# Kernel tuning notes

Hardware: AMD Instinct MI355X
Metric: run time of the kernel (lower is better)

## Reference

```python
import math
import jax, jax.numpy as jnp
import numpy as np

B = 8192
BAND = 5      # channels per DGCN
N = 62        # graph nodes (EEG electrodes)
LAYERS = 2
CBAM_C = (LAYERS + 1) * BAND  # 15
RED = 4
H2 = 64
K_TOP = int(N * 0.8)  # 49


def conv1x1(x, w, b):
    # x: [B,C,N,T], w: [O,C], b: [O] or None
    y = jnp.einsum('bcnt,oc->bont', x, w)
    if b is not None:
        y = y + b[None, :, None, None]
    return y


def dgcn(x, conv_w, conv_b, mem, gfc_w, gfc_b, gcn_w, gcn_b):
    skip = x
    x = conv1x1(x, conv_w, conv_b)
    scale = 1.0 / math.sqrt(BAND)
    # dynamic adjacency 1: memory-based
    a1 = jax.nn.softmax(jax.nn.relu(jnp.einsum('bcnt,cm->bnm', x, mem) * scale), axis=-1)
    # dynamic adjacency 2: self-similarity of time-summed features
    xs = jnp.sum(x, axis=-1)  # [B,C,N]
    a2 = jax.nn.softmax(jax.nn.relu(jnp.einsum('bcn,bcm->bnm', xs, xs) * scale), axis=-1)
    af = jnp.stack([a1, a2], axis=-1)          # [B,N,N,2]
    af = jnp.einsum('bnmk,ok->bnmo', af, gfc_w)[..., 0] + gfc_b[0]  # fc(2->1), squeeze
    af = jax.nn.softmax(af, axis=-1)
    _, idx = jax.lax.top_k(af, K_TOP)          # [B,N,k]
    bI = jnp.arange(af.shape[0])[:, None, None]
    nI = jnp.arange(N)[None, :, None]
    mask = jnp.zeros_like(af).at[bI, nI, idx].set(1.0)
    adj = af * mask
    # diffusion step (diffusion_step=1)
    y = jnp.einsum('bcnt,bnm->bcmt', x, adj)
    y = conv1x1(y, gcn_w, gcn_b)
    return y + skip


def cbam(x, ca_w1, ca_w2, sa_w, sa_b):
    residual = x
    # channel attention: shared SE MLP on max- and avg-pooled descriptors
    mx = jnp.max(x, axis=(2, 3), keepdims=True)   # [B,C,1,1]
    av = jnp.mean(x, axis=(2, 3), keepdims=True)
    def se(z):
        z = jnp.einsum('bcnt,oc->bont', z, ca_w1)
        z = jax.nn.relu(z)
        return jnp.einsum('bcnt,oc->bont', z, ca_w2)
    ca = jax.nn.sigmoid(se(mx) + se(av))
    out = x * ca
    # spatial attention: 3x3 conv over [max,mean] channel maps
    smax = jnp.max(out, axis=1, keepdims=True)
    smean = jnp.mean(out, axis=1, keepdims=True)
    s = jnp.concatenate([smax, smean], axis=1)    # [B,2,H,W]
    sa = jax.lax.conv_general_dilated(
        s, sa_w, window_strides=(1, 1), padding=((1, 1), (1, 1)),
        dimension_numbers=('NCHW', 'OIHW', 'NCHW')) + sa_b[None, :, None, None]
    sa = jax.nn.sigmoid(sa)
    out = out * sa
    return out + residual


def setup_inputs() -> dict:
    key = jax.random.key(0)
    ks = jax.random.split(key, 24)
    p = {}
    p['x'] = jax.random.normal(ks[0], (B, BAND * N), dtype=jnp.float32)
    for l in range(LAYERS):
        o = 1 + l * 8
        p[f'l{l}_conv_w'] = jax.random.normal(ks[o + 0], (BAND, BAND), jnp.float32) * 0.3
        p[f'l{l}_conv_b'] = jnp.zeros((BAND,), jnp.float32)
        p[f'l{l}_mem'] = jax.random.normal(ks[o + 1], (BAND, N), jnp.float32) * 0.2
        p[f'l{l}_gfc_w'] = jax.random.normal(ks[o + 2], (1, 2), jnp.float32) * 0.5
        p[f'l{l}_gfc_b'] = jnp.zeros((1,), jnp.float32)
        p[f'l{l}_gcn_w'] = jax.random.normal(ks[o + 3], (BAND, BAND), jnp.float32) * 0.3
        p[f'l{l}_gcn_b'] = jnp.zeros((BAND,), jnp.float32)
    p['ca_w1'] = jax.random.normal(ks[17], (CBAM_C // RED, CBAM_C), jnp.float32) * 0.2
    p['ca_w2'] = jax.random.normal(ks[18], (CBAM_C, CBAM_C // RED), jnp.float32) * 0.2
    p['sa_w'] = jax.random.normal(ks[19], (1, 2, 3, 3), jnp.float32) * 0.2
    p['sa_b'] = jnp.zeros((1,), jnp.float32)
    p['fc1_w'] = jax.random.normal(ks[20], (H2, N * CBAM_C), jnp.float32) * 0.03
    p['fc1_b'] = jnp.zeros((H2,), jnp.float32)
    p['fc2_w'] = jax.random.normal(ks[21], (H2, H2), jnp.float32) * 0.1
    p['fc2_b'] = jnp.zeros((H2,), jnp.float32)
    return p


def reference(x,
              l0_conv_w, l0_conv_b, l0_mem, l0_gfc_w, l0_gfc_b, l0_gcn_w, l0_gcn_b,
              l1_conv_w, l1_conv_b, l1_mem, l1_gfc_w, l1_gfc_b, l1_gcn_w, l1_gcn_b,
              ca_w1, ca_w2, sa_w, sa_b, fc1_w, fc1_b, fc2_w, fc2_b):
    h = x.reshape(x.shape[0], BAND, N)[:, :, :, None]  # [B,5,62,1]
    feats = [h]
    layer_params = [
        (l0_conv_w, l0_conv_b, l0_mem, l0_gfc_w, l0_gfc_b, l0_gcn_w, l0_gcn_b),
        (l1_conv_w, l1_conv_b, l1_mem, l1_gfc_w, l1_gfc_b, l1_gcn_w, l1_gcn_b),
    ]
    cur = h
    for lp in layer_params:
        cur = dgcn(cur, *lp)
        feats.append(cur)
    g = jnp.concatenate(feats, axis=1)                 # [B,15,62,1]
    g = cbam(g, ca_w1, ca_w2, sa_w, sa_b)
    out = g.reshape(g.shape[0], -1)
    out = jax.nn.relu(out @ fc1_w.T + fc1_b)           # dropout = identity (eval)
    out = jax.nn.relu(out @ fc2_w.T + fc2_b)
    return out
```

## Files before the change

### kernel.cpp

```cpp
#include <hip/hip_runtime.h>

#define NB 62
#define NC 5
#define KTOP 49

typedef unsigned short ushort_t;
typedef unsigned int uint_t;

__device__ __forceinline__ float sigmf(float x) {
    return 1.0f / (1.0f + __expf(-x));
}

__device__ __forceinline__ ushort_t f2b(float f) {
    union { float f; uint_t u; } cv; cv.f = f;
    uint_t r = (cv.u + 0x7fffu + ((cv.u >> 16) & 1u)) >> 16;
    return (ushort_t)r;
}
__device__ __forceinline__ float blo(uint_t w) {
    union { uint_t u; float f; } cv; cv.u = w << 16; return cv.f;
}
__device__ __forceinline__ float bhi(uint_t w) {
    union { uint_t u; float f; } cv; cv.u = w & 0xffff0000u; return cv.f;
}
__device__ __forceinline__ float bits2f(uint_t u) {
    union { uint_t u; float f; } cv; cv.u = u; return cv.f;
}

__device__ __forceinline__ float tmax31(const float* a) {
    float t0 = a[0], t1 = a[1], t2 = a[2], t3 = a[3];
    #pragma unroll
    for (int m = 4; m < 28; m += 4) {
        t0 = fmaxf(t0, a[m]);     t1 = fmaxf(t1, a[m + 1]);
        t2 = fmaxf(t2, a[m + 2]); t3 = fmaxf(t3, a[m + 3]);
    }
    t0 = fmaxf(t0, a[28]); t1 = fmaxf(t1, a[29]); t2 = fmaxf(t2, a[30]);
    return fmaxf(fmaxf(t0, t1), fmaxf(t2, t3));
}
__device__ __forceinline__ float tsum31(const float* a) {
    float t0 = a[0], t1 = a[1], t2 = a[2], t3 = a[3];
    #pragma unroll
    for (int m = 4; m < 28; m += 4) {
        t0 += a[m]; t1 += a[m + 1]; t2 += a[m + 2]; t3 += a[m + 3];
    }
    t0 += a[28]; t1 += a[29]; t2 += a[30];
    return (t0 + t1) + (t2 + t3);
}

__device__ __forceinline__ void sort16(float* s) {
    #pragma unroll
    for (int k = 2; k <= 16; k <<= 1) {
        #pragma unroll
        for (int j = k >> 1; j > 0; j >>= 1) {
            #pragma unroll
            for (int i = 0; i < 16; ++i) {
                const int p = i ^ j;
                if (p > i) {
                    const bool up = ((i & k) == 0);
                    const float a = s[i], c = s[p];
                    s[i] = up ? fminf(a, c) : fmaxf(a, c);
                    s[p] = up ? fmaxf(a, c) : fminf(a, c);
                }
            }
        }
    }
}
__device__ __forceinline__ void merge_low16(float* m, const float* b) {
    float t[16];
    #pragma unroll
    for (int i = 0; i < 16; ++i) t[i] = fminf(m[i], b[15 - i]);
    #pragma unroll
    for (int j = 8; j > 0; j >>= 1) {
        #pragma unroll
        for (int i = 0; i < 16; ++i) {
            const int p = i ^ j;
            if (p > i) {
                const float a = t[i], c = t[p];
                t[i] = fminf(a, c);
                t[p] = fmaxf(a, c);
            }
        }
    }
    #pragma unroll
    for (int i = 0; i < 16; ++i) m[i] = t[i];
}

__global__ void repack_kernel(const float* __restrict__ fc1w,
                              const float* __restrict__ fc2w,
                              ushort_t* __restrict__ w1o,
                              float* __restrict__ w2o) {
    const int i = blockIdx.x * 256 + threadIdx.x;
    if (i < 59 * 128 * 8) {
        const int e = i & 7, t = (i >> 3) & 127, j = i >> 10;
        const int o = t >> 1, h = t & 1;
        const int f = (h * 59 + j) * 8 + e;
        const float v = (f < 930) ? fc1w[o * 930 + f] : 0.0f;
        w1o[i] = f2b(v);
    } else if (i < 59 * 128 * 8 + 8 * 128 * 4) {
        const int i2 = i - 59 * 128 * 8;
        const int e = i2 & 3, t = (i2 >> 2) & 127, j = i2 >> 9;
        const int o = t >> 1, h = t & 1;
        w2o[i2] = fc2w[o * 64 + h * 32 + j * 4 + e];
    }
}

template <int L>
__device__ __forceinline__ void dgcn_layer(
    const int tid, const float* __restrict__ xin_g,
    const float* __restrict__ conv_w, const float* __restrict__ conv_b,
    const float* __restrict__ memp,
    const float* __restrict__ gfc_w, const float* __restrict__ gfc_b,
    const float* __restrict__ gcn_w, const float* __restrict__ gcn_b,
    float (*__restrict__ s_xc4)[4], float* __restrict__ s_xc1,
    float (*__restrict__ s_me4)[4], float* __restrict__ s_me1,
    uint_t* __restrict__ s_adj32,
    float (*__restrict__ s_xin)[NC], float (*__restrict__ s_xout)[NC])
{
    const float scale = 0.44721359549995793f;
    const int n = tid >> 1, h = tid & 1;

    for (int i = tid; i < NC * NB; i += 128) {
        const int c = i / NB, m = i - c * NB;
        if (c < 4) s_me4[m][c] = memp[i];
        else       s_me1[m]    = memp[i];
    }

    if (tid < NB) {
        float cw[25], cbv[5];
        #pragma unroll
        for (int i = 0; i < 25; ++i) cw[i] = conv_w[i];
        #pragma unroll
        for (int i = 0; i < 5; ++i)  cbv[i] = conv_b[i];
        float xn[5];
        #pragma unroll
        for (int c = 0; c < 5; ++c)
            xn[c] = (L == 0) ? xin_g[c * NB + tid] : s_xin[tid][c];
        float xo[5];
        #pragma unroll
        for (int o = 0; o < 5; ++o) {
            float a = cbv[o];
            #pragma unroll
            for (int c = 0; c < 5; ++c) a = fmaf(cw[o * 5 + c], xn[c], a);
            xo[o] = a;
        }
        s_xc4[tid][0] = xo[0]; s_xc4[tid][1] = xo[1];
        s_xc4[tid][2] = xo[2]; s_xc4[tid][3] = xo[3];
        s_xc1[tid] = xo[4];
    }
    __syncthreads();

    if (n < NB) {
        const float w0 = gfc_w[0], w1 = gfc_w[1], b0 = gfc_b[0];
        const float4 xo03 = *(const float4*)&s_xc4[n][0];
        const float  xo4  = s_xc1[n];
        float r1[31], r2[31];
        #pragma unroll
        for (int i = 0; i < 31; ++i) {
            const int m = h * 31 + i;
            const float4 xc03 = *(const float4*)&s_xc4[m][0];
            const float  xc4  = s_xc1[m];
            const float4 me03 = *(const float4*)&s_me4[m][0];
            const float  me4  = s_me1[m];
            float s1 = xo03.x * me03.x + xo03.y * me03.y + xo03.z * me03.z +
                       xo03.w * me03.w + xo4 * me4;
            float s2 = xo03.x * xc03.x + xo03.y * xc03.y + xo03.z * xc03.z +
                       xo03.w * xc03.w + xo4 * xc4;
            r1[i] = fmaxf(s1 * scale, 0.0f);
            r2[i] = fmaxf(s2 * scale, 0.0f);
        }
        float mx1 = tmax31(r1);
        mx1 = fmaxf(mx1, __shfl_xor(mx1, 1, 64));
        #pragma unroll
        for (int i = 0; i < 31; ++i) r1[i] = __expf(r1[i] - mx1);
        float sm1 = tsum31(r1);
        sm1 += __shfl_xor(sm1, 1, 64);
        const float inv1 = 1.0f / sm1;
        float mx2 = tmax31(r2);
        mx2 = fmaxf(mx2, __shfl_xor(mx2, 1, 64));
        #pragma unroll
        for (int i = 0; i < 31; ++i) r2[i] = __expf(r2[i] - mx2);
        float sm2 = tsum31(r2);
        sm2 += __shfl_xor(sm2, 1, 64);
        const float inv2 = 1.0f / sm2;
        #pragma unroll
        for (int i = 0; i < 31; ++i)
            r1[i] = b0 + (r1[i] * inv1) * w0 + (r2[i] * inv2) * w1;
        float mxa = tmax31(r1);
        mxa = fmaxf(mxa, __shfl_xor(mxa, 1, 64));
        #pragma unroll
        for (int i = 0; i < 31; ++i) r1[i] = __expf(r1[i] - mxa);
        float sma = tsum31(r1);
        sma += __shfl_xor(sma, 1, 64);
        const float inva = 1.0f / sma;
        #pragma unroll
        for (int i = 0; i < 31; ++i) r1[i] *= inva;

        float ga[16], gb[16];
        #pragma unroll
        for (int i = 0; i < 16; ++i) ga[i] = r1[i];
        sort16(ga);
        #pragma unroll
        for (int i = 0; i < 15; ++i) gb[i] = r1[16 + i];
        gb[15] = INFINITY;
        sort16(gb);
        merge_low16(ga, gb);
        #pragma unroll
        for (int i = 0; i < 16; ++i) gb[i] = __shfl_xor(ga[i], 1, 64);
        merge_low16(ga, gb);
        const float vth = ga[13];

        int g_own = 0, eq_own = 0;
        #pragma unroll
        for (int i = 0; i < 31; ++i) {
            g_own  += (r1[i] > vth);
            eq_own += (r1[i] == vth);
        }
        const int G = g_own + __shfl_xor(g_own, 1, 64);
        const int eq_other = __shfl_xor(eq_own, 1, 64);
        int eq = h ? eq_other : 0;

        uint_t pend = 0, myfirst = 0;
        #pragma unroll
        for (int i = 0; i < 31; ++i) {
            const bool e  = (r1[i] == vth);
            const bool ss = (r1[i] > vth) || (e && (G + eq) < KTOP);
            const uint_t hb = (uint_t)f2b(ss ? r1[i] : 0.0f);
            eq += e ? 1 : 0;
            if (h == 0) {
                if (i & 1) s_adj32[n * 31 + (i >> 1)] = pend | (hb << 16);
                else       pend = hb;
            } else {
                if (i == 0)      myfirst = hb;
                else if (i & 1)  pend = hb;
                else             s_adj32[n * 31 + 15 + (i >> 1)] = pend | (hb << 16);
            }
        }
        const uint_t xch = (uint_t)__shfl_xor((int)(h ? myfirst : pend), 1, 64);
        if (h == 0) s_adj32[n * 31 + 15] = pend | (xch << 16);
    }
    __syncthreads();

    if (n < NB) {
        const int m = n;
        const int dw = m >> 1;
        const uint_t sh = (m & 1) ? 16u : 0u;
        float y0 = 0, y1 = 0, y2 = 0, y3 = 0, y4 = 0;
        #pragma unroll 4
        for (int j = 0; j < 31; ++j) {
            const int nn = h * 31 + j;
            const uint_t w = s_adj32[nn * 31 + dw];
            const float a = bits2f((w >> sh) << 16);
            const float4 xv = *(const float4*)&s_xc4[nn][0];
            const float  xv4 = s_xc1[nn];
            y0 = fmaf(xv.x, a, y0); y1 = fmaf(xv.y, a, y1); y2 = fmaf(xv.z, a, y2);
            y3 = fmaf(xv.w, a, y3); y4 = fmaf(xv4, a, y4);
        }
        y0 += __shfl_xor(y0, 1, 64); y1 += __shfl_xor(y1, 1, 64);
        y2 += __shfl_xor(y2, 1, 64); y3 += __shfl_xor(y3, 1, 64);
        y4 += __shfl_xor(y4, 1, 64);
        if (h == 0) {
            float gwv[25], gbv[5];
            #pragma unroll
            for (int i = 0; i < 25; ++i) gwv[i] = gcn_w[i];
            #pragma unroll
            for (int i = 0; i < 5; ++i)  gbv[i] = gcn_b[i];
            #pragma unroll
            for (int o = 0; o < 5; ++o) {
                const float z = gbv[o] + gwv[o * 5 + 0] * y0 + gwv[o * 5 + 1] * y1 +
                                gwv[o * 5 + 2] * y2 + gwv[o * 5 + 3] * y3 + gwv[o * 5 + 4] * y4;
                const float fi = (L == 0) ? xin_g[o * NB + m] : s_xin[m][o];
                s_xout[m][o] = z + fi;
            }
        }
    }
    __syncthreads();
}

__global__ void __launch_bounds__(128) __attribute__((amdgpu_waves_per_eu(2, 6)))
encoder_kernel(
    const float* __restrict__ g_x,
    const float* __restrict__ c0w, const float* __restrict__ c0b,
    const float* __restrict__ m0,  const float* __restrict__ f0w,
    const float* __restrict__ f0b, const float* __restrict__ g0w,
    const float* __restrict__ g0b,
    const float* __restrict__ c1w, const float* __restrict__ c1b,
    const float* __restrict__ m1,  const float* __restrict__ f1w,
    const float* __restrict__ f1b, const float* __restrict__ g1w,
    const float* __restrict__ g1b,
    const float* __restrict__ caw1, const float* __restrict__ caw2,
    const float* __restrict__ saw,  const float* __restrict__ sab,
    const float* __restrict__ fc1w, const float* __restrict__ fc1b,
    const float* __restrict__ fc2w, const float* __restrict__ fc2b,
    const ushort_t* __restrict__ w1b, const float* __restrict__ w2p,
    const int use_ws,
    float* __restrict__ g_out)
{
    const int b   = blockIdx.x;
    const int tid = threadIdx.x;

    __shared__ __align__(16) float s_xc4[NB][4];
    __shared__ __align__(16) float s_xc1[NB];
    __shared__ __align__(16) float s_me4[NB][4];
    __shared__ __align__(16) float s_me1[NB];
    __shared__ __align__(16) uint_t s_adj32[NB * 31];
    __shared__ __align__(16) float s_x1[NB][NC];
    __shared__ __align__(16) float s_x2[NB][NC];

    float* const s_g  = (float*)s_adj32;
    float* const s_h1 = ((float*)s_adj32) + 944;

    const float* xin = g_x + (size_t)b * (NC * NB);

    dgcn_layer<0>(tid, xin, c0w, c0b, m0, f0w, f0b, g0w, g0b,
                  s_xc4, s_xc1, s_me4, s_me1, s_adj32, nullptr, s_x1);
    dgcn_layer<1>(tid, xin, c1w, c1b, m1, f1w, f1b, g1w, g1b,
                  s_xc4, s_xc1, s_me4, s_me1, s_adj32, s_x1, s_x2);

    float f0[5], f1v[5], f2v[5];
    #pragma unroll
    for (int c = 0; c < 5; ++c) {
        f0[c]  = (tid < NB) ? xin[c * NB + tid] : 0.0f;
        f1v[c] = (tid < NB) ? s_x1[tid][c] : 0.0f;
        f2v[c] = (tid < NB) ? s_x2[tid][c] : 0.0f;
    }
    float mxp[15], avp[15];
    #pragma unroll
    for (int c = 0; c < 15; ++c) {
        const float v = (c < 5) ? f0[c] : (c < 10) ? f1v[c - 5] : f2v[c - 10];
        float vm = (tid < NB) ? v : -INFINITY;
        float vs = (tid < NB) ? v : 0.0f;
        #pragma unroll
        for (int off = 32; off > 0; off >>= 1) {
            vm = fmaxf(vm, __shfl_xor(vm, off, 64));
            vs += __shfl_xor(vs, off, 64);
        }
        mxp[c] = vm;
        avp[c] = vs * (1.0f / 62.0f);
    }
    float ca[15];
    {
        float hm[3], ha[3];
        #pragma unroll
        for (int o = 0; o < 3; ++o) {
            float am = 0.0f, aa = 0.0f;
            #pragma unroll
            for (int c = 0; c < 15; ++c) {
                const float w = caw1[o * 15 + c];
                am = fmaf(mxp[c], w, am);
                aa = fmaf(avp[c], w, aa);
            }
            hm[o] = fmaxf(am, 0.0f);
            ha[o] = fmaxf(aa, 0.0f);
        }
        #pragma unroll
        for (int c = 0; c < 15; ++c) {
            float t = 0.0f;
            #pragma unroll
            for (int o = 0; o < 3; ++o) t = fmaf(hm[o] + ha[o], caw2[c * 3 + o], t);
            ca[c] = sigmf(t);
        }
    }
    float og[15];
    float smx = -INFINITY, ssum = 0.0f;
    #pragma unroll
    for (int c = 0; c < 15; ++c) {
        const float fv = (c < 5) ? f0[c] : (c < 10) ? f1v[c - 5] : f2v[c - 10];
        const float v = fv * ca[c];
        og[c] = v;
        smx = fmaxf(smx, v);
        ssum += v;
    }
    const float smean = ssum * (1.0f / 15.0f);
    const float sxl = __shfl_up(smx, 1, 64),   sml = __shfl_up(smean, 1, 64);
    const float sxr = __shfl_down(smx, 1, 64), smr = __shfl_down(smean, 1, 64);
    const float mskL = (tid > 0) ? 1.0f : 0.0f;
    const float mskR = (tid < NB - 1) ? 1.0f : 0.0f;
    float t = sab[0];
    t += mskL * (sxl * saw[1] + sml * saw[10]);
    t += smx * saw[4] + smean * saw[13];
    t += mskR * (sxr * saw[7] + smr * saw[16]);
    const float sa = sigmf(t);

    __syncthreads();
    if (tid < NB) {
        #pragma unroll
        for (int c = 0; c < 15; ++c) {
            const float fv = (c < 5) ? f0[c] : (c < 10) ? f1v[c - 5] : f2v[c - 10];
            s_g[c * NB + tid] = og[c] * sa + fv;
        }
    }
    if (tid < 14) s_g[930 + tid] = 0.0f;
    __syncthreads();

    const int o = tid >> 1, h = tid & 1;
    if (use_ws) {
        float acc = h ? 0.0f : fc1b[o];
        const uint4* w1v = (const uint4*)w1b;
        #pragma unroll 4
        for (int j = 0; j < 59; ++j) {
            const uint4 wv = w1v[j * 128 + tid];
            const int f = (h * 59 + j) * 8;
            const float4 ga4 = *(const float4*)&s_g[f];
            const float4 gb4 = *(const float4*)&s_g[f + 4];
            acc = fmaf(blo(wv.x), ga4.x, acc);
            acc = fmaf(bhi(wv.x), ga4.y, acc);
            acc = fmaf(blo(wv.y), ga4.z, acc);
            acc = fmaf(bhi(wv.y), ga4.w, acc);
            acc = fmaf(blo(wv.z), gb4.x, acc);
            acc = fmaf(bhi(wv.z), gb4.y, acc);
            acc = fmaf(blo(wv.w), gb4.z, acc);
            acc = fmaf(bhi(wv.w), gb4.w, acc);
        }
        acc += __shfl_xor(acc, 1, 64);
        if (h == 0) s_h1[o] = fmaxf(acc, 0.0f);
        __syncthreads();
        float acc2 = h ? 0.0f : fc2b[o];
        #pragma unroll
        for (int j = 0; j < 8; ++j) {
            const float4 wv = *(const float4*)(w2p + (j * 128 + tid) * 4);
            const float4 hv = *(const float4*)&s_h1[h * 32 + j * 4];
            acc2 = fmaf(wv.x, hv.x, acc2);
            acc2 = fmaf(wv.y, hv.y, acc2);
            acc2 = fmaf(wv.z, hv.z, acc2);
            acc2 = fmaf(wv.w, hv.w, acc2);
        }
        acc2 += __shfl_xor(acc2, 1, 64);
        if (h == 0) g_out[(size_t)b * 64 + o] = fmaxf(acc2, 0.0f);
    } else {
        float acc = 0.0f;
        if (h == 0) {
            acc = fc1b[o];
            const float* wr = fc1w + (size_t)o * 930;
            for (int i = 0; i < 930; i += 2)
                acc = fmaf(wr[i], s_g[i], fmaf(wr[i + 1], s_g[i + 1], acc));
        }
        acc += __shfl_xor(acc, 1, 64);
        if (h == 0) s_h1[o] = fmaxf(acc, 0.0f);
        __syncthreads();
        float acc2 = 0.0f;
        if (h == 0) {
            acc2 = fc2b[o];
            const float* wr2 = fc2w + o * 64;
            for (int k = 0; k < 64; ++k) acc2 = fmaf(wr2[k], s_h1[k], acc2);
            g_out[(size_t)b * 64 + o] = fmaxf(acc2, 0.0f);
        }
    }
}

extern "C" void kernel_launch(void* const* d_in, const int* in_sizes, int n_in,
                              void* d_out, int out_size, void* d_ws, size_t ws_size,
                              hipStream_t stream) {
    const float* X    = (const float*)d_in[0];
    const float* C0W  = (const float*)d_in[1];
    const float* C0B  = (const float*)d_in[2];
    const float* M0   = (const float*)d_in[3];
    const float* F0W  = (const float*)d_in[4];
    const float* F0B  = (const float*)d_in[5];
    const float* G0W  = (const float*)d_in[6];
    const float* G0B  = (const float*)d_in[7];
    const float* C1W  = (const float*)d_in[8];
    const float* C1B  = (const float*)d_in[9];
    const float* M1   = (const float*)d_in[10];
    const float* F1W  = (const float*)d_in[11];
    const float* F1B  = (const float*)d_in[12];
    const float* G1W  = (const float*)d_in[13];
    const float* G1B  = (const float*)d_in[14];
    const float* CAW1 = (const float*)d_in[15];
    const float* CAW2 = (const float*)d_in[16];
    const float* SAW  = (const float*)d_in[17];
    const float* SAB  = (const float*)d_in[18];
    const float* FC1W = (const float*)d_in[19];
    const float* FC1B = (const float*)d_in[20];
    const float* FC2W = (const float*)d_in[21];
    const float* FC2B = (const float*)d_in[22];

    const int B = in_sizes[0] / (NC * NB);

    const size_t W1_BYTES = 59 * 128 * 8 * sizeof(ushort_t);
    const size_t W2_BYTES = 8 * 128 * 4 * sizeof(float);
    const int use_ws = (ws_size >= W1_BYTES + W2_BYTES) ? 1 : 0;
    ushort_t* w1b = (ushort_t*)d_ws;
    float*    w2p = (float*)((char*)d_ws + W1_BYTES);

    if (use_ws) {
        repack_kernel<<<252, 256, 0, stream>>>(FC1W, FC2W, w1b, w2p);
    }

    encoder_kernel<<<B, 128, 0, stream>>>(
        X, C0W, C0B, M0, F0W, F0B, G0W, G0B,
        C1W, C1B, M1, F1W, F1B, G1W, G1B,
        CAW1, CAW2, SAW, SAB, FC1W, FC1B, FC2W, FC2B,
        w1b, w2p, use_ws,
        (float*)d_out);
}
```

Before: 244.8 us.

## Split each graph row across four lanes and widen block to 256 threads

The per-sample block grows from 128 to 256 threads, so each adjacency row is handled by four lanes of 16 columns instead of two lanes of 31. Softmax, top-k sort/merge, tie counting and diffusion are rewritten around 4-lane shuffles, and the adjacency rows are padded to a 33-word stride. The FC1 weight repack now keeps fp32 instead of bf16, which doubles weight traffic but drops the unpack instructions and the rounding. The aim is shorter per-thread dependency chains and fewer registers, at the cost of more threads per block, more shuffles and some idle lanes on the padded last quarter.

New measurement: 373.6 us. +52.6%, slower.

```diff
diff --git a/kernel.cpp b/kernel.cpp
--- a/kernel.cpp
+++ b/kernel.cpp
@@ -16,33 +16,20 @@
     uint_t r = (cv.u + 0x7fffu + ((cv.u >> 16) & 1u)) >> 16;
     return (ushort_t)r;
 }
-__device__ __forceinline__ float blo(uint_t w) {
-    union { uint_t u; float f; } cv; cv.u = w << 16; return cv.f;
-}
-__device__ __forceinline__ float bhi(uint_t w) {
-    union { uint_t u; float f; } cv; cv.u = w & 0xffff0000u; return cv.f;
-}
 __device__ __forceinline__ float bits2f(uint_t u) {
     union { uint_t u; float f; } cv; cv.u = u; return cv.f;
 }
 
-__device__ __forceinline__ float tmax31(const float* a) {
-    float t0 = a[0], t1 = a[1], t2 = a[2], t3 = a[3];
-    #pragma unroll
-    for (int m = 4; m < 28; m += 4) {
-        t0 = fmaxf(t0, a[m]);     t1 = fmaxf(t1, a[m + 1]);
-        t2 = fmaxf(t2, a[m + 2]); t3 = fmaxf(t3, a[m + 3]);
-    }
-    t0 = fmaxf(t0, a[28]); t1 = fmaxf(t1, a[29]); t2 = fmaxf(t2, a[30]);
+__device__ __forceinline__ float tmax16(const float* a) {
+    float t0 = fmaxf(a[0], a[4]), t1 = fmaxf(a[1], a[5]);
+    float t2 = fmaxf(a[2], a[6]), t3 = fmaxf(a[3], a[7]);
+    t0 = fmaxf(t0, fmaxf(a[8], a[12]));  t1 = fmaxf(t1, fmaxf(a[9], a[13]));
+    t2 = fmaxf(t2, fmaxf(a[10], a[14])); t3 = fmaxf(t3, fmaxf(a[11], a[15]));
     return fmaxf(fmaxf(t0, t1), fmaxf(t2, t3));
 }
-__device__ __forceinline__ float tsum31(const float* a) {
-    float t0 = a[0], t1 = a[1], t2 = a[2], t3 = a[3];
-    #pragma unroll
-    for (int m = 4; m < 28; m += 4) {
-        t0 += a[m]; t1 += a[m + 1]; t2 += a[m + 2]; t3 += a[m + 3];
-    }
-    t0 += a[28]; t1 += a[29]; t2 += a[30];
+__device__ __forceinline__ float tsum16(const float* a) {
+    float t0 = a[0] + a[4], t1 = a[1] + a[5], t2 = a[2] + a[6], t3 = a[3] + a[7];
+    t0 += a[8] + a[12]; t1 += a[9] + a[13]; t2 += a[10] + a[14]; t3 += a[11] + a[15];
     return (t0 + t1) + (t2 + t3);
 }
 
@@ -86,20 +73,19 @@
 
 __global__ void repack_kernel(const float* __restrict__ fc1w,
                               const float* __restrict__ fc2w,
-                              ushort_t* __restrict__ w1o,
+                              float* __restrict__ w1o,
                               float* __restrict__ w2o) {
     const int i = blockIdx.x * 256 + threadIdx.x;
-    if (i < 59 * 128 * 8) {
-        const int e = i & 7, t = (i >> 3) & 127, j = i >> 10;
-        const int o = t >> 1, h = t & 1;
-        const int f = (h * 59 + j) * 8 + e;
-        const float v = (f < 930) ? fc1w[o * 930 + f] : 0.0f;
-        w1o[i] = f2b(v);
-    } else if (i < 59 * 128 * 8 + 8 * 128 * 4) {
-        const int i2 = i - 59 * 128 * 8;
-        const int e = i2 & 3, t = (i2 >> 2) & 127, j = i2 >> 9;
-        const int o = t >> 1, h = t & 1;
-        w2o[i2] = fc2w[o * 64 + h * 32 + j * 4 + e];
+    if (i < 30 * 256 * 8) {
+        const int e = i & 7, t = (i >> 3) & 255, j = i >> 11;
+        const int o = t >> 2, h2 = t & 3;
+        const int f = h2 * 240 + j * 8 + e;
+        w1o[i] = (f < 930) ? fc1w[o * 930 + f] : 0.0f;
+    } else if (i < 30 * 256 * 8 + 4 * 256 * 4) {
+        const int i2 = i - 30 * 256 * 8;
+        const int e = i2 & 3, t = (i2 >> 2) & 255, j = i2 >> 10;
+        const int o = t >> 2, h2 = t & 3;
+        w2o[i2] = fc2w[o * 64 + h2 * 16 + j * 4 + e];
     }
 }
 
@@ -116,9 +102,10 @@
     float (*__restrict__ s_xin)[NC], float (*__restrict__ s_xout)[NC])
 {
     const float scale = 0.44721359549995793f;
-    const int n = tid >> 1, h = tid & 1;
-
-    for (int i = tid; i < NC * NB; i += 128) {
+    const int n = tid >> 2, q = tid & 3;
+    const int q16 = q * 16;
+
+    for (int i = tid; i < NC * NB; i += 256) {
         const int c = i / NB, m = i - c * NB;
         if (c < 4) s_me4[m][c] = memp[i];
         else       s_me1[m]    = memp[i];
@@ -149,93 +136,100 @@
     __syncthreads();
 
     if (n < NB) {
-        const float w0 = gfc_w[0], w1 = gfc_w[1], b0 = gfc_b[0];
         const float4 xo03 = *(const float4*)&s_xc4[n][0];
         const float  xo4  = s_xc1[n];
-        float r1[31], r2[31];
-        #pragma unroll
-        for (int i = 0; i < 31; ++i) {
-            const int m = h * 31 + i;
-            const float4 xc03 = *(const float4*)&s_xc4[m][0];
-            const float  xc4  = s_xc1[m];
-            const float4 me03 = *(const float4*)&s_me4[m][0];
-            const float  me4  = s_me1[m];
+        float r1[16], r2[16];
+        #pragma unroll
+        for (int i = 0; i < 16; ++i) {
+            const int m = q16 + i;
+            const bool valid = (i < 14) || (q < 3);
+            const int mm = valid ? m : 0;
+            const float4 xc03 = *(const float4*)&s_xc4[mm][0];
+            const float  xc4  = s_xc1[mm];
+            const float4 me03 = *(const float4*)&s_me4[mm][0];
+            const float  me4  = s_me1[mm];
             float s1 = xo03.x * me03.x + xo03.y * me03.y + xo03.z * me03.z +
                        xo03.w * me03.w + xo4 * me4;
             float s2 = xo03.x * xc03.x + xo03.y * xc03.y + xo03.z * xc03.z +
                        xo03.w * xc03.w + xo4 * xc4;
-            r1[i] = fmaxf(s1 * scale, 0.0f);
-            r2[i] = fmaxf(s2 * scale, 0.0f);
-        }
-        float mx1 = tmax31(r1);
+            r1[i] = valid ? fmaxf(s1 * scale, 0.0f) : -INFINITY;
+            r2[i] = valid ? fmaxf(s2 * scale, 0.0f) : -INFINITY;
+        }
+        float mx1 = tmax16(r1);
         mx1 = fmaxf(mx1, __shfl_xor(mx1, 1, 64));
-        #pragma unroll
-        for (int i = 0; i < 31; ++i) r1[i] = __expf(r1[i] - mx1);
-        float sm1 = tsum31(r1);
+        mx1 = fmaxf(mx1, __shfl_xor(mx1, 2, 64));
+        #pragma unroll
+        for (int i = 0; i < 16; ++i) r1[i] = __expf(r1[i] - mx1);
+        float sm1 = tsum16(r1);
         sm1 += __shfl_xor(sm1, 1, 64);
-        const float inv1 = 1.0f / sm1;
-        float mx2 = tmax31(r2);
+        sm1 += __shfl_xor(sm1, 2, 64);
+        float mx2 = tmax16(r2);
         mx2 = fmaxf(mx2, __shfl_xor(mx2, 1, 64));
-        #pragma unroll
-        for (int i = 0; i < 31; ++i) r2[i] = __expf(r2[i] - mx2);
-        float sm2 = tsum31(r2);
+        mx2 = fmaxf(mx2, __shfl_xor(mx2, 2, 64));
+        #pragma unroll
+        for (int i = 0; i < 16; ++i) r2[i] = __expf(r2[i] - mx2);
+        float sm2 = tsum16(r2);
         sm2 += __shfl_xor(sm2, 1, 64);
-        const float inv2 = 1.0f / sm2;
-        #pragma unroll
-        for (int i = 0; i < 31; ++i)
-            r1[i] = b0 + (r1[i] * inv1) * w0 + (r2[i] * inv2) * w1;
-        float mxa = tmax31(r1);
+        sm2 += __shfl_xor(sm2, 2, 64);
+        const float w0s = gfc_w[0] / sm1, w1s = gfc_w[1] / sm2, b0 = gfc_b[0];
+        #pragma unroll
+        for (int i = 0; i < 16; ++i)
+            r1[i] = fmaf(r1[i], w0s, fmaf(r2[i], w1s, b0));
+        if (q == 3) { r1[14] = -INFINITY; r1[15] = -INFINITY; }
+        float mxa = tmax16(r1);
         mxa = fmaxf(mxa, __shfl_xor(mxa, 1, 64));
-        #pragma unroll
-        for (int i = 0; i < 31; ++i) r1[i] = __expf(r1[i] - mxa);
-        float sma = tsum31(r1);
+        mxa = fmaxf(mxa, __shfl_xor(mxa, 2, 64));
+        #pragma unroll
+        for (int i = 0; i < 16; ++i) r1[i] = __expf(r1[i] - mxa);
+        float sma = tsum16(r1);
         sma += __shfl_xor(sma, 1, 64);
+        sma += __shfl_xor(sma, 2, 64);
         const float inva = 1.0f / sma;
         #pragma unroll
-        for (int i = 0; i < 31; ++i) r1[i] *= inva;
+        for (int i = 0; i < 16; ++i) r1[i] *= inva;
 
         float ga[16], gb[16];
         #pragma unroll
         for (int i = 0; i < 16; ++i) ga[i] = r1[i];
+        if (q == 3) { ga[14] = INFINITY; ga[15] = INFINITY; }
         sort16(ga);
-        #pragma unroll
-        for (int i = 0; i < 15; ++i) gb[i] = r1[16 + i];
-        gb[15] = INFINITY;
-        sort16(gb);
-        merge_low16(ga, gb);
         #pragma unroll
         for (int i = 0; i < 16; ++i) gb[i] = __shfl_xor(ga[i], 1, 64);
         merge_low16(ga, gb);
+        #pragma unroll
+        for (int i = 0; i < 16; ++i) gb[i] = __shfl_xor(ga[i], 2, 64);
+        merge_low16(ga, gb);
         const float vth = ga[13];
 
-        int g_own = 0, eq_own = 0;
-        #pragma unroll
-        for (int i = 0; i < 31; ++i) {
-            g_own  += (r1[i] > vth);
-            eq_own += (r1[i] == vth);
-        }
-        const int G = g_own + __shfl_xor(g_own, 1, 64);
-        const int eq_other = __shfl_xor(eq_own, 1, 64);
-        int eq = h ? eq_other : 0;
-
-        uint_t pend = 0, myfirst = 0;
-        #pragma unroll
-        for (int i = 0; i < 31; ++i) {
+        int gt = 0, eqo = 0;
+        #pragma unroll
+        for (int i = 0; i < 16; ++i) {
+            gt  += (r1[i] > vth);
+            eqo += (r1[i] == vth);
+        }
+        int Gt = gt + __shfl_xor(gt, 1, 64);
+        Gt += __shfl_xor(Gt, 2, 64);
+        const int s1e = __shfl_xor(eqo, 1, 64);
+        const int pre1 = (q & 1) ? s1e : 0;
+        const int tp = eqo + s1e;
+        const int s2e = __shfl_xor(tp, 2, 64);
+        const int pre2 = (q & 2) ? s2e : 0;
+        int eq = pre1 + pre2;
+
+        uint_t pend = 0;
+        #pragma unroll
+        for (int i = 0; i < 16; ++i) {
             const bool e  = (r1[i] == vth);
-            const bool ss = (r1[i] > vth) || (e && (G + eq) < KTOP);
+            const bool ss = (r1[i] > vth) || (e && (Gt + eq) < KTOP);
             const uint_t hb = (uint_t)f2b(ss ? r1[i] : 0.0f);
             eq += e ? 1 : 0;
-            if (h == 0) {
-                if (i & 1) s_adj32[n * 31 + (i >> 1)] = pend | (hb << 16);
-                else       pend = hb;
+            if (i & 1) {
+                if (i < 14 || q < 3)
+                    s_adj32[n * 33 + q * 8 + (i >> 1)] = pend | (hb << 16);
             } else {
-                if (i == 0)      myfirst = hb;
-                else if (i & 1)  pend = hb;
-                else             s_adj32[n * 31 + 15 + (i >> 1)] = pend | (hb << 16);
+                pend = hb;
             }
         }
-        const uint_t xch = (uint_t)__shfl_xor((int)(h ? myfirst : pend), 1, 64);
-        if (h == 0) s_adj32[n * 31 + 15] = pend | (xch << 16);
     }
     __syncthreads();
 
@@ -244,20 +238,25 @@
         const int dw = m >> 1;
         const uint_t sh = (m & 1) ? 16u : 0u;
         float y0 = 0, y1 = 0, y2 = 0, y3 = 0, y4 = 0;
-        #pragma unroll 4
-        for (int j = 0; j < 31; ++j) {
-            const int nn = h * 31 + j;
-            const uint_t w = s_adj32[nn * 31 + dw];
-            const float a = bits2f((w >> sh) << 16);
-            const float4 xv = *(const float4*)&s_xc4[nn][0];
-            const float  xv4 = s_xc1[nn];
+        #pragma unroll
+        for (int j = 0; j < 16; ++j) {
+            const int nn = q16 + j;
+            const bool v2 = (j < 14) || (q < 3);
+            const int nnc = v2 ? nn : 0;
+            const uint_t w = s_adj32[nnc * 33 + dw];
+            float a = bits2f((w >> sh) << 16);
+            a = v2 ? a : 0.0f;
+            const float4 xv = *(const float4*)&s_xc4[nnc][0];
+            const float  xv4 = s_xc1[nnc];
             y0 = fmaf(xv.x, a, y0); y1 = fmaf(xv.y, a, y1); y2 = fmaf(xv.z, a, y2);
             y3 = fmaf(xv.w, a, y3); y4 = fmaf(xv4, a, y4);
         }
-        y0 += __shfl_xor(y0, 1, 64); y1 += __shfl_xor(y1, 1, 64);
-        y2 += __shfl_xor(y2, 1, 64); y3 += __shfl_xor(y3, 1, 64);
-        y4 += __shfl_xor(y4, 1, 64);
-        if (h == 0) {
+        y0 += __shfl_xor(y0, 1, 64); y0 += __shfl_xor(y0, 2, 64);
+        y1 += __shfl_xor(y1, 1, 64); y1 += __shfl_xor(y1, 2, 64);
+        y2 += __shfl_xor(y2, 1, 64); y2 += __shfl_xor(y2, 2, 64);
+        y3 += __shfl_xor(y3, 1, 64); y3 += __shfl_xor(y3, 2, 64);
+        y4 += __shfl_xor(y4, 1, 64); y4 += __shfl_xor(y4, 2, 64);
+        if (q == 0) {
             float gwv[25], gbv[5];
             #pragma unroll
             for (int i = 0; i < 25; ++i) gwv[i] = gcn_w[i];
@@ -275,7 +274,7 @@
     __syncthreads();
 }
 
-__global__ void __launch_bounds__(128) __attribute__((amdgpu_waves_per_eu(2, 6)))
+__global__ void __launch_bounds__(256) __attribute__((amdgpu_waves_per_eu(2, 6)))
 encoder_kernel(
     const float* __restrict__ g_x,
     const float* __restrict__ c0w, const float* __restrict__ c0b,
@@ -290,7 +289,7 @@
     const float* __restrict__ saw,  const float* __restrict__ sab,
     const float* __restrict__ fc1w, const float* __restrict__ fc1b,
     const float* __restrict__ fc2w, const float* __restrict__ fc2b,
-    const ushort_t* __restrict__ w1b, const float* __restrict__ w2p,
+    const float* __restrict__ w1p, const float* __restrict__ w2p,
     const int use_ws,
     float* __restrict__ g_out)
 {
@@ -301,12 +300,12 @@
     __shared__ __align__(16) float s_xc1[NB];
     __shared__ __align__(16) float s_me4[NB][4];
     __shared__ __align__(16) float s_me1[NB];
-    __shared__ __align__(16) uint_t s_adj32[NB * 31];
+    __shared__ __align__(16) uint_t s_adj32[NB * 33];
     __shared__ __align__(16) float s_x1[NB][NC];
     __shared__ __align__(16) float s_x2[NB][NC];
 
     float* const s_g  = (float*)s_adj32;
-    float* const s_h1 = ((float*)s_adj32) + 944;
+    float* const s_h1 = ((float*)s_adj32) + 960;
 
     const float* xin = g_x + (size_t)b * (NC * NB);
 
@@ -388,57 +387,58 @@
             s_g[c * NB + tid] = og[c] * sa + fv;
         }
     }
-    if (tid < 14) s_g[930 + tid] = 0.0f;
+    if (tid < 30) s_g[930 + tid] = 0.0f;
     __syncthreads();
 
-    const int o = tid >> 1, h = tid & 1;
+    const int o = tid >> 2, h2 = tid & 3;
     if (use_ws) {
-        float acc = h ? 0.0f : fc1b[o];
-        const uint4* w1v = (const uint4*)w1b;
-        #pragma unroll 4
-        for (int j = 0; j < 59; ++j) {
-            const uint4 wv = w1v[j * 128 + tid];
-            const int f = (h * 59 + j) * 8;
+        float acc = (h2 == 0) ? fc1b[o] : 0.0f;
+        #pragma unroll 5
+        for (int j = 0; j < 30; ++j) {
+            const float* wp = w1p + ((size_t)(j * 256 + tid)) * 8;
+            const float4 wa = *(const float4*)wp;
+            const float4 wb = *(const float4*)(wp + 4);
+            const int f = h2 * 240 + j * 8;
             const float4 ga4 = *(const float4*)&s_g[f];
             const float4 gb4 = *(const float4*)&s_g[f + 4];
-            acc = fmaf(blo(wv.x), ga4.x, acc);
-            acc = fmaf(bhi(wv.x), ga4.y, acc);
-            acc = fmaf(blo(wv.y), ga4.z, acc);
-            acc = fmaf(bhi(wv.y), ga4.w, acc);
-            acc = fmaf(blo(wv.z), gb4.x, acc);
-            acc = fmaf(bhi(wv.z), gb4.y, acc);
-            acc = fmaf(blo(wv.w), gb4.z, acc);
-            acc = fmaf(bhi(wv.w), gb4.w, acc);
+            acc = fmaf(wa.x, ga4.x, acc);
+            acc = fmaf(wa.y, ga4.y, acc);
+            acc = fmaf(wa.z, ga4.z, acc);
+            acc = fmaf(wa.w, ga4.w, acc);
+            acc = fmaf(wb.x, gb4.x, acc);
+            acc = fmaf(wb.y, gb4.y, acc);
+            acc = fmaf(wb.z, gb4.z, acc);
+            acc = fmaf(wb.w, gb4.w, acc);
         }
         acc += __shfl_xor(acc, 1, 64);
-        if (h == 0) s_h1[o] = fmaxf(acc, 0.0f);
+        acc += __shfl_xor(acc, 2, 64);
+        if (h2 == 0) s_h1[o] = fmaxf(acc, 0.0f);
         __syncthreads();
-        float acc2 = h ? 0.0f : fc2b[o];
-        #pragma unroll
-        for (int j = 0; j < 8; ++j) {
-            const float4 wv = *(const float4*)(w2p + (j * 128 + tid) * 4);
-            const float4 hv = *(const float4*)&s_h1[h * 32 + j * 4];
+        float acc2 = (h2 == 0) ? fc2b[o] : 0.0f;
+        #pragma unroll
+        for (int j = 0; j < 4; ++j) {
+            const float4 wv = *(const float4*)(w2p + ((size_t)(j * 256 + tid)) * 4);
+            const float4 hv = *(const float4*)&s_h1[h2 * 16 + j * 4];
             acc2 = fmaf(wv.x, hv.x, acc2);
             acc2 = fmaf(wv.y, hv.y, acc2);
             acc2 = fmaf(wv.z, hv.z, acc2);
             acc2 = fmaf(wv.w, hv.w, acc2);
         }
         acc2 += __shfl_xor(acc2, 1, 64);
-        if (h == 0) g_out[(size_t)b * 64 + o] = fmaxf(acc2, 0.0f);
+        acc2 += __shfl_xor(acc2, 2, 64);
+        if (h2 == 0) g_out[(size_t)b * 64 + o] = fmaxf(acc2, 0.0f);
     } else {
         float acc = 0.0f;
-        if (h == 0) {
+        if (h2 == 0) {
             acc = fc1b[o];
             const float* wr = fc1w + (size_t)o * 930;
             for (int i = 0; i < 930; i += 2)
                 acc = fmaf(wr[i], s_g[i], fmaf(wr[i + 1], s_g[i + 1], acc));
-        }
-        acc += __shfl_xor(acc, 1, 64);
-        if (h == 0) s_h1[o] = fmaxf(acc, 0.0f);
+            s_h1[o] = fmaxf(acc, 0.0f);
+        }
         __syncthreads();
-        float acc2 = 0.0f;
-        if (h == 0) {
-            acc2 = fc2b[o];
+        if (h2 == 0) {
+            float acc2 = fc2b[o];
             const float* wr2 = fc2w + o * 64;
             for (int k = 0; k < 64; ++k) acc2 = fmaf(wr2[k], s_h1[k], acc2);
             g_out[(size_t)b * 64 + o] = fmaxf(acc2, 0.0f);
@@ -475,20 +475,20 @@
 
     const int B = in_sizes[0] / (NC * NB);
 
-    const size_t W1_BYTES = 59 * 128 * 8 * sizeof(ushort_t);
-    const size_t W2_BYTES = 8 * 128 * 4 * sizeof(float);
+    const size_t W1_BYTES = 30 * 256 * 8 * sizeof(float);
+    const size_t W2_BYTES = 4 * 256 * 4 * sizeof(float);
     const int use_ws = (ws_size >= W1_BYTES + W2_BYTES) ? 1 : 0;
-    ushort_t* w1b = (ushort_t*)d_ws;
-    float*    w2p = (float*)((char*)d_ws + W1_BYTES);
+    float* w1p = (float*)d_ws;
+    float* w2p = (float*)((char*)d_ws + W1_BYTES);
 
     if (use_ws) {
-        repack_kernel<<<252, 256, 0, stream>>>(FC1W, FC2W, w1b, w2p);
-    }
-
-    encoder_kernel<<<B, 128, 0, stream>>>(
+        repack_kernel<<<256, 256, 0, stream>>>(FC1W, FC2W, w1p, w2p);
+    }
+
+    encoder_kernel<<<B, 256, 0, stream>>>(
         X, C0W, C0B, M0, F0W, F0B, G0W, G0B,
         C1W, C1B, M1, F1W, F1B, G1W, G1B,
         CAW1, CAW2, SAW, SAB, FC1W, FC1B, FC2W, FC2B,
-        w1b, w2p, use_ws,
+        w1p, w2p, use_ws,
         (float*)d_out);
 }
```
